# Performance work log

Measured on AMD Instinct MI355X. Metric: run time of the kernel, lower is better.

Reference implementation:

```python
import jax, jax.numpy as jnp
import numpy as np
import math

B, M, D = 16, 2048, 512
H, K, NB = 8, 5, 5
HD = D // H
FF = 2048


def _p(key, shape, scale=0.02):
    return (jax.random.normal(key, shape, dtype=jnp.float32) * scale)


def setup_inputs() -> dict:
    key = jax.random.key(0)
    ks = jax.random.split(key, 16)
    inp = {
        'x': jax.random.normal(ks[0], (B, M, D), dtype=jnp.float32),
        'mask': jnp.ones((B, 1, M), dtype=bool),
        'ln1_g': jnp.ones((D,), jnp.float32), 'ln1_b': jnp.zeros((D,), jnp.float32),
        'Wk': _p(ks[1], (D, D)), 'bk': jnp.zeros((D,), jnp.float32),
        'Wv': _p(ks[2], (D, D)), 'bv': jnp.zeros((D,), jnp.float32),
        'Wq': _p(ks[3], (D, D)), 'bq': jnp.zeros((D,), jnp.float32),
        'Woff': _p(ks[4], (D, H * K)), 'boff': jnp.zeros((H * K,), jnp.float32),
        'Wo': _p(ks[5], (D, D)), 'bo': jnp.zeros((D,), jnp.float32),
        'ln2_g': jnp.ones((D,), jnp.float32), 'ln2_b': jnp.zeros((D,), jnp.float32),
        'W1': _p(ks[6], (D, FF)), 'b1': jnp.zeros((FF,), jnp.float32),
        'W2': _p(ks[7], (FF, D)), 'b2': jnp.zeros((D,), jnp.float32),
    }
    return inp


def layer_norm(x, g, b, eps=1e-6):
    mu = jnp.mean(x, axis=-1, keepdims=True)
    var = jnp.mean((x - mu) ** 2, axis=-1, keepdims=True)
    return (x - mu) / jnp.sqrt(var + eps) * g + b


def grid_sample_1d(src, gx):
    # src: [BH, Min, hd], gx: [BH, M, K] normalized x-coords in [-1,1]
    # Replicates torch grid_sample(bilinear, zeros, align_corners=False) with
    # H_in=1 and y-grid==1 -> implicit 0.5 factor from y-interp against zero pad.
    BH, Min, hd = src.shape
    ix = ((gx + 1.0) * Min - 1.0) / 2.0
    x0 = jnp.floor(ix)
    w1 = ix - x0
    x0i = x0.astype(jnp.int32)

    def gather(xi):
        valid = ((xi >= 0) & (xi < Min)).astype(src.dtype)
        xc = jnp.clip(xi, 0, Min - 1)
        flat = xc.reshape(BH, -1)
        vals = jnp.take_along_axis(src, flat[:, :, None], axis=1)
        return vals.reshape(BH, xi.shape[1], xi.shape[2], hd) * valid[..., None]

    v0 = gather(x0i)
    v1 = gather(x0i + 1)
    return ((1.0 - w1)[..., None] * v0 + w1[..., None] * v1) * 0.5


def reference(x, mask, ln1_g, ln1_b, Wk, bk, Wv, bv, Wq, bq, Woff, boff,
              Wo, bo, ln2_g, ln2_b, W1, b1, W2, b2):
    Bs, Ms, Ds = x.shape
    xn = layer_norm(x, ln1_g, ln1_b)
    k = xn @ Wk + bk
    v = xn @ Wv + bv
    q = xn @ Wq + bq

    # query_type == 'mean': AvgPool1d(kernel=NB, stride=1, pad=NB//2),
    # count_include_pad=True -> moving sum over zero-padded seq / NB
    pad = NB // 2
    qp = jnp.pad(q, ((0, 0), (pad, pad), (0, 0)))
    cs = jnp.concatenate([jnp.zeros((Bs, 1, Ds), q.dtype), jnp.cumsum(qp, axis=1)], axis=1)
    q = (cs[:, NB:, :] - cs[:, :-NB, :]) / float(NB)  # [B, M, D]

    offsets = (q @ Woff + boff).reshape(Bs, Ms, H, K).transpose(0, 2, 1, 3)  # [B,H,M,K]
    kh = k.reshape(Bs, Ms, H, HD).transpose(0, 2, 1, 3)  # [B,H,M,hd]
    vh = v.reshape(Bs, Ms, H, HD).transpose(0, 2, 1, 3)
    qh = q.reshape(Bs, Ms, H, HD).transpose(0, 2, 1, 3)

    loc = jnp.arange(Ms, dtype=jnp.float32)[:, None]          # [M,1]
    left = -K // 2                                            # Python floor div: -3 for K=5
    ref = jnp.arange(left, K + left, dtype=jnp.float32)       # [K]
    sign_lens = jnp.squeeze(jnp.sum(mask, axis=-1)).astype(jnp.float32) - 1.0  # [B]

    sl = ref + offsets + loc                                  # [B,H,M,K]
    sl = jnp.mod(sl, sign_lens[:, None, None, None])
    gx = (sl / (Ms - 1) * 2.0 - 1.0).reshape(Bs * H, Ms, K)

    ksrc = kh.reshape(Bs * H, Ms, HD)
    vsrc = vh.reshape(Bs * H, Ms, HD)
    sk = grid_sample_1d(ksrc, gx).reshape(Bs, H, Ms, K, HD)
    sv = grid_sample_1d(vsrc, gx).reshape(Bs, H, Ms, K, HD)

    qh = qh / math.sqrt(HD)
    scores = jnp.einsum('bhmd,bhmkd->bhmk', qh, sk)
    attn = jax.nn.softmax(scores, axis=-1)
    ctx = jnp.einsum('bhmk,bhmkd->bhmd', attn, sv)
    ctx = ctx.transpose(0, 2, 1, 3).reshape(Bs, Ms, H * HD)
    att_out = ctx @ Wo + bo

    o = att_out + x  # dropout=0.0
    on = layer_norm(o, ln2_g, ln2_b)
    ff = jax.nn.relu(on @ W1 + b1) @ W2 + b2
    return ff + o
```

## Files before the change

### kernel.cpp

```cpp
#include <hip/hip_runtime.h>


#define B_   16
#define M_   2048
#define D_   512
#define H_   8
#define K_   5
#define HD_  64
#define FF_  2048
#define NROWS (B_ * M_)

typedef unsigned short u16;
typedef __attribute__((ext_vector_type(4))) unsigned short u16x4;
typedef __attribute__((ext_vector_type(8))) unsigned short u16x8;
typedef __attribute__((ext_vector_type(8))) short short8;
typedef __attribute__((ext_vector_type(4))) float f32x4;

__device__ __forceinline__ u16 f2bf(float f) {
  unsigned u = __builtin_bit_cast(unsigned, f);
  u += 0x7fff + ((u >> 16) & 1);
  return (u16)(u >> 16);
}
__device__ __forceinline__ float bf2f(u16 h) {
  unsigned u = (unsigned)h << 16;
  return __builtin_bit_cast(float, u);
}

#define GLP(p)  ((__attribute__((address_space(1))) void*)(p))
#define LDSP(p) ((__attribute__((address_space(3))) void*)(p))

__global__ __launch_bounds__(256)
void wtrans(const float* __restrict__ in, int K, int N,
            u16* __restrict__ out, int padN) {
  __shared__ float t[32][33];
  const int tx = threadIdx.x, ty = threadIdx.y;
  const int n0 = blockIdx.x * 32, k0 = blockIdx.y * 32;
#pragma unroll
  for (int r = 0; r < 4; ++r) {
    const int k = k0 + ty + r * 8;
    const int n = n0 + tx;
    t[ty + r * 8][tx] = (n < N) ? in[(size_t)k * N + n] : 0.f;
  }
  __syncthreads();
#pragma unroll
  for (int r = 0; r < 4; ++r) {
    const int nn = n0 + ty + r * 8;
    out[(size_t)nn * K + k0 + tx] = f2bf(t[tx][ty + r * 8]);
  }
}

__global__ __launch_bounds__(256)
void kvperm(const u16* __restrict__ tmp, u16* __restrict__ out) {
  const int g = blockIdx.x * 256 + threadIdx.x;
  const int row = g >> 6, j = g & 63;
  const int h = row >> 7, r = row & 127;
  const int src = ((r >> 2) & 1) * 512 + h * 64 + (r >> 3) * 4 + (r & 3);
  *(u16x8*)&out[(size_t)row * 512 + j * 8] =
      *(const u16x8*)&tmp[(size_t)src * 512 + j * 8];
}

__global__ __launch_bounds__(256)
void bias_cat(const float* __restrict__ bk, const float* __restrict__ bv,
              const float* __restrict__ bq, float* __restrict__ o) {
  const int i = blockIdx.x * 256 + threadIdx.x;
  if (i >= 1024) { o[i] = bq[i - 1024]; return; }
  const int h = i >> 7, r = i & 127;
  const int c = h * 64 + (r >> 3) * 4 + (r & 3);
  o[i] = ((r >> 2) & 1) ? bv[c] : bk[c];
}

__global__ __launch_bounds__(128)
void ln_bf16(const float* __restrict__ x, const float* __restrict__ g,
             const float* __restrict__ bsh, u16* __restrict__ y) {
  const int row = blockIdx.x;
  float4 v = ((const float4*)(x + (size_t)row * D_))[threadIdx.x];
  float s  = v.x + v.y + v.z + v.w;
  float s2 = v.x * v.x + v.y * v.y + v.z * v.z + v.w * v.w;
#pragma unroll
  for (int off = 32; off; off >>= 1) {
    s  += __shfl_xor(s, off);
    s2 += __shfl_xor(s2, off);
  }
  __shared__ float sh[4];
  if ((threadIdx.x & 63) == 0) {
    sh[threadIdx.x >> 6]       = s;
    sh[2 + (threadIdx.x >> 6)] = s2;
  }
  __syncthreads();
  s = sh[0] + sh[1]; s2 = sh[2] + sh[3];
  const float mu  = s * (1.0f / D_);
  const float var = s2 * (1.0f / D_) - mu * mu;
  const float inv = rsqrtf(var + 1e-6f);
  float4 gv = ((const float4*)g)[threadIdx.x];
  float4 bv = ((const float4*)bsh)[threadIdx.x];
  u16x4 o;
  o.x = f2bf((v.x - mu) * inv * gv.x + bv.x);
  o.y = f2bf((v.y - mu) * inv * gv.y + bv.y);
  o.z = f2bf((v.z - mu) * inv * gv.z + bv.z);
  o.w = f2bf((v.w - mu) * inv * gv.w + bv.w);
  *(u16x4*)(y + (size_t)row * D_ + threadIdx.x * 4) = o;
}

__global__ __launch_bounds__(128)
void ln_bf16_in(const u16* __restrict__ x, const float* __restrict__ g,
                const float* __restrict__ bsh, u16* __restrict__ y) {
  const int row = blockIdx.x;
  u16x4 hv = *(const u16x4*)(x + (size_t)row * D_ + threadIdx.x * 4);
  float4 v;
  v.x = bf2f(hv.x); v.y = bf2f(hv.y); v.z = bf2f(hv.z); v.w = bf2f(hv.w);
  float s  = v.x + v.y + v.z + v.w;
  float s2 = v.x * v.x + v.y * v.y + v.z * v.z + v.w * v.w;
#pragma unroll
  for (int off = 32; off; off >>= 1) {
    s  += __shfl_xor(s, off);
    s2 += __shfl_xor(s2, off);
  }
  __shared__ float sh[4];
  if ((threadIdx.x & 63) == 0) {
    sh[threadIdx.x >> 6]       = s;
    sh[2 + (threadIdx.x >> 6)] = s2;
  }
  __syncthreads();
  s = sh[0] + sh[1]; s2 = sh[2] + sh[3];
  const float mu  = s * (1.0f / D_);
  const float var = s2 * (1.0f / D_) - mu * mu;
  const float inv = rsqrtf(var + 1e-6f);
  float4 gv = ((const float4*)g)[threadIdx.x];
  float4 bv = ((const float4*)bsh)[threadIdx.x];
  u16x4 o;
  o.x = f2bf((v.x - mu) * inv * gv.x + bv.x);
  o.y = f2bf((v.y - mu) * inv * gv.y + bv.y);
  o.z = f2bf((v.z - mu) * inv * gv.z + bv.z);
  o.w = f2bf((v.w - mu) * inv * gv.w + bv.w);
  *(u16x4*)(y + (size_t)row * D_ + threadIdx.x * 4) = o;
}

template<int EPI, int OUTBF, int RBF>
__global__ __launch_bounds__(512, 2)
void mgemmS(const u16* __restrict__ A, int lda,
            const u16* __restrict__ Wt, int ldb, int Kdim,
            const float* __restrict__ bias,
            const void* R, int ldr,
            void* Cv, int ldc, int Ncols, int nbx) {
  __shared__ u16 lds[81920] __attribute__((aligned(128)));
  int bid = blockIdx.x;
  { const int q = (int)gridDim.x >> 3; bid = (bid & 7) * q + (bid >> 3); }
  const int bx = bid % nbx, by = bid / nbx;
  const int m0 = by * 256, n0 = bx * 256;

  const int tid  = threadIdx.x;
  const int w    = tid >> 6, lane = tid & 63;
  const int wr   = w >> 2,   wc   = w & 3;
  const int lr   = lane & 15, kg  = lane >> 4;
  const int NT   = Kdim >> 6;
  const int srow = (w << 3) + (lane >> 3);
  const int scol = (((lane & 7) ^ (lane >> 3)) << 3);

  const u16* Ab = A  + (size_t)m0 * lda;
  const u16* Bb = Wt + (size_t)n0 * ldb;

  auto stage = [&](const u16* gbase, int ld, int kt, int h, int base) {
    const u16* s0 = gbase + (size_t)(h * 128 + srow) * ld + kt * 64 + scol;
    const u16* s1 = s0 + (size_t)64 * ld;
    u16* d0 = &lds[base + h * 8192 + w * 512];
    __builtin_amdgcn_global_load_lds(GLP(s0), LDSP(d0),        16, 0, 0);
    __builtin_amdgcn_global_load_lds(GLP(s1), LDSP(d0 + 4096), 16, 0, 0);
  };
  auto rdA = [&](int base, int f, int s) -> short8 {
    const int row = wr * 128 + f * 16 + lr;
    const int cb  = (kg * 16 + s * 64) ^ ((lr & 7) << 4);
    return *(const short8*)&lds[base + row * 64 + (cb >> 1)];
  };
  auto rdB = [&](int bsel, int nn, int s) -> short8 {
    const int row = wc * 64 + nn * 16 + lr;
    const int cb  = (kg * 16 + s * 64) ^ ((lr & 7) << 4);
    return *(const short8*)&lds[49152 + bsel * 16384 + row * 64 + (cb >> 1)];
  };

  f32x4 acc[8][4];
#pragma unroll
  for (int f = 0; f < 8; ++f)
#pragma unroll
    for (int n = 0; n < 4; ++n) acc[f][n] = (f32x4){0.f, 0.f, 0.f, 0.f};

  stage(Ab, lda, 0, 0, 0);      stage(Ab, lda, 0, 1, 0);
  stage(Bb, ldb, 0, 0, 49152);  stage(Bb, ldb, 0, 1, 49152);
  if (NT > 1) {
    stage(Ab, lda, 1, 0, 16384);  stage(Ab, lda, 1, 1, 16384);
    stage(Bb, ldb, 1, 0, 65536);  stage(Bb, ldb, 1, 1, 65536);
    asm volatile("s_waitcnt vmcnt(8)" ::: "memory");
  } else {
    asm volatile("s_waitcnt vmcnt(0)" ::: "memory");
  }
  asm volatile("s_barrier" ::: "memory");

  int aCur = 0, bCur = 0;
  for (int t = 0; t < NT; ++t) {
    int aT2 = aCur + 2; if (aT2 >= 3) aT2 -= 3;
    const int aBase = aCur * 16384;
    const int aT2b  = aT2 * 16384;
    const int bT2b  = 49152 + bCur * 16384;
    short8 bfr[4][2];
    short8 afr[2][2][2];
#pragma unroll
    for (int n = 0; n < 4; ++n) { bfr[n][0] = rdB(bCur, n, 0); bfr[n][1] = rdB(bCur, n, 1); }
#pragma unroll
    for (int i = 0; i < 2; ++i) { afr[0][i][0] = rdA(aBase, i, 0); afr[0][i][1] = rdA(aBase, i, 1); }
    if (t + 2 < NT) { stage(Ab, lda, t + 2, 0, aT2b); stage(Ab, lda, t + 2, 1, aT2b); }
#pragma unroll
    for (int q = 0; q < 4; ++q) {
      if (q < 3) {
#pragma unroll
        for (int i = 0; i < 2; ++i) {
          afr[(q + 1) & 1][i][0] = rdA(aBase, 2 * (q + 1) + i, 0);
          afr[(q + 1) & 1][i][1] = rdA(aBase, 2 * (q + 1) + i, 1);
        }
      }
#pragma unroll
      for (int i = 0; i < 2; ++i)
#pragma unroll
        for (int n = 0; n < 4; ++n) {
          acc[2 * q + i][n] = __builtin_amdgcn_mfma_f32_16x16x32_bf16(afr[q & 1][i][0], bfr[n][0], acc[2 * q + i][n], 0, 0, 0);
          acc[2 * q + i][n] = __builtin_amdgcn_mfma_f32_16x16x32_bf16(afr[q & 1][i][1], bfr[n][1], acc[2 * q + i][n], 0, 0, 0);
        }
      if (q == 0) {
        asm volatile("s_waitcnt lgkmcnt(8)" ::: "memory");
        asm volatile("s_barrier" ::: "memory");
        if (t + 2 < NT) { stage(Bb, ldb, t + 2, 0, bT2b); stage(Bb, ldb, t + 2, 1, bT2b); }
      }
    }
    if (t + 1 < NT) {
      if (t + 2 < NT) { asm volatile("s_waitcnt vmcnt(8) lgkmcnt(0)" ::: "memory"); }
      else            { asm volatile("s_waitcnt vmcnt(0) lgkmcnt(0)" ::: "memory"); }
      asm volatile("s_barrier" ::: "memory");
    }
    aCur = (aCur + 1 < 3) ? aCur + 1 : 0;
    bCur ^= 1;
  }

  float* eplds = (float*)lds;
  asm volatile("s_waitcnt vmcnt(0) lgkmcnt(0)" ::: "memory");
  __builtin_amdgcn_s_barrier();
  const int ccol = lane * 4;
  float4 bb4 = make_float4(0.f, 0.f, 0.f, 0.f);
  if (n0 + ccol < Ncols) bb4 = *(const float4*)(bias + n0 + ccol);
#pragma unroll
  for (int half = 0; half < 2; ++half) {
#pragma unroll
    for (int fl = 0; fl < 4; ++fl) {
      const int f  = half * 4 + fl;
      const int cr = (fl * 2 + wr) * 16 + kg * 4;
#pragma unroll
      for (int n = 0; n < 4; ++n)
#pragma unroll
        for (int r = 0; r < 4; ++r)
          eplds[(cr + r) * 260 + wc * 64 + n * 16 + lr] = acc[f][n][r];
    }
    asm volatile("s_waitcnt lgkmcnt(0)" ::: "memory");
    __builtin_amdgcn_s_barrier();
#pragma unroll
    for (int i = 0; i < 16; ++i) {
      const int cr  = w * 16 + i;
      const int fl2 = cr >> 5, wr2 = (cr >> 4) & 1, r16 = cr & 15;
      const int grow = m0 + wr2 * 128 + (half * 4 + fl2) * 16 + r16;
      const int gcol = n0 + ccol;
      if (gcol < Ncols) {
        float4 v = *(const float4*)&eplds[cr * 260 + ccol];
        v.x += bb4.x; v.y += bb4.y; v.z += bb4.z; v.w += bb4.w;
        if (EPI == 1) {
          if (RBF) {
            u16x4 rv = *(const u16x4*)((const u16*)R + (size_t)grow * ldr + gcol);
            v.x += bf2f(rv.x); v.y += bf2f(rv.y); v.z += bf2f(rv.z); v.w += bf2f(rv.w);
          } else {
            float4 rv = *(const float4*)((const float*)R + (size_t)grow * ldr + gcol);
            v.x += rv.x; v.y += rv.y; v.z += rv.z; v.w += rv.w;
          }
        }
        if (EPI == 2) {
          v.x = fmaxf(v.x, 0.f); v.y = fmaxf(v.y, 0.f);
          v.z = fmaxf(v.z, 0.f); v.w = fmaxf(v.w, 0.f);
        }
        if (OUTBF) {
          u16x4 o;
          o.x = f2bf(v.x); o.y = f2bf(v.y); o.z = f2bf(v.z); o.w = f2bf(v.w);
          *(u16x4*)((u16*)Cv + (size_t)grow * ldc + gcol) = o;
        } else {
          *(float4*)((float*)Cv + (size_t)grow * ldc + gcol) = v;
        }
      }
    }
    if (half == 0) {
      asm volatile("s_waitcnt lgkmcnt(0)" ::: "memory");
      __builtin_amdgcn_s_barrier();
    }
  }
}

__global__ __launch_bounds__(256)
void pool_q_bf(const u16* __restrict__ kvq, u16* __restrict__ qp) {
  const size_t idx = (size_t)blockIdx.x * 256 + threadIdx.x;
  const int d4 = (int)(idx & 127);
  const size_t bm = idx >> 7;
  const int m = (int)(bm & (M_ - 1));
  float a0 = 0.f, a1 = 0.f, a2 = 0.f, a3 = 0.f;
#pragma unroll
  for (int j = -2; j <= 2; ++j) {
    const int mm = m + j;
    if (mm >= 0 && mm < M_) {
      u16x4 tv = *(const u16x4*)(kvq + (bm + j) * 1536 + 1024 + d4 * 4);
      a0 += bf2f(tv.x); a1 += bf2f(tv.y); a2 += bf2f(tv.z); a3 += bf2f(tv.w);
    }
  }
  u16x4 o;
  o.x = f2bf(a0 * 0.2f); o.y = f2bf(a1 * 0.2f);
  o.z = f2bf(a2 * 0.2f); o.w = f2bf(a3 * 0.2f);
  *(u16x4*)(qp + bm * D_ + d4 * 4) = o;
}

__global__ __launch_bounds__(256)
void attn3(const u16* __restrict__ KVQ, const u16* __restrict__ QP,
           const float* __restrict__ OFFS, u16* __restrict__ CTX) {
  const int tid  = threadIdx.x;
  const int lane = tid & 63;
  const int j    = lane & 7;
  const int grp  = lane >> 3;
  const int gid  = blockIdx.x * 32 + (tid >> 6) * 8 + grp;
  const int m  = gid & (M_ - 1);
  const int bh = gid >> 11;
  const int h  = bh & (H_ - 1);
  const int b  = bh >> 3;
  const size_t bm = (size_t)b * M_ + m;

  float qs[8];
  {
    u16x8 qv = *(const u16x8*)(QP + bm * D_ + h * HD_ + j * 8);
#pragma unroll
    for (int e = 0; e < 8; ++e) qs[e] = bf2f(qv[e]) * 0.0625f;
  }
  const float* ob = OFFS + bm * (H_ * K_) + h * K_;
  const u16* kvb = KVQ + h * 128 + j * 16;
  const size_t rowb = (size_t)b * M_;

  float sc[K_], sv[K_][8];
#pragma unroll
  for (int kk = 0; kk < K_; ++kk) {
    float sl = (float)(m + kk - 3) + ob[kk];
    if (sl < 0.f) sl += 2047.f;
    else if (sl >= 2047.f) sl -= 2047.f;
    const float ix  = sl * (2048.0f / 2047.0f) - 0.5f;
    const float x0f = floorf(ix);
    const float w1  = ix - x0f;
    const int   x0  = (int)x0f;
    u16x8 a0, b0, a1, b1;
#pragma unroll
    for (int e = 0; e < 8; ++e) { a0[e] = 0; b0[e] = 0; a1[e] = 0; b1[e] = 0; }
    if (x0 >= 0) {
      const u16* p = kvb + (rowb + x0) * 1536;
      a0 = *(const u16x8*)p; b0 = *(const u16x8*)(p + 8);
    }
    if (x0 < M_ - 1) {
      const u16* p = kvb + (rowb + x0 + 1) * 1536;
      a1 = *(const u16x8*)p; b1 = *(const u16x8*)(p + 8);
    }
    float part = 0.f;
#pragma unroll
    for (int e = 0; e < 4; ++e) {
      const float k0 = bf2f(a0[e]),     k1 = bf2f(a1[e]);
      const float v0 = bf2f(a0[e + 4]), v1 = bf2f(a1[e + 4]);
      part += (k0 + w1 * (k1 - k0)) * qs[e];
      sv[kk][e] = v0 + w1 * (v1 - v0);
      const float k0b = bf2f(b0[e]),     k1b = bf2f(b1[e]);
      const float v0b = bf2f(b0[e + 4]), v1b = bf2f(b1[e + 4]);
      part += (k0b + w1 * (k1b - k0b)) * qs[e + 4];
      sv[kk][e + 4] = v0b + w1 * (v1b - v0b);
    }
    part += __shfl_xor(part, 1);
    part += __shfl_xor(part, 2);
    part += __shfl_xor(part, 4);
    sc[kk] = part;
  }
  float mx = sc[0];
#pragma unroll
  for (int kk = 1; kk < K_; ++kk) mx = fmaxf(mx, sc[kk]);
  float den = 0.f;
#pragma unroll
  for (int kk = 0; kk < K_; ++kk) { sc[kk] = __expf(sc[kk] - mx); den += sc[kk]; }
  const float inv = 1.0f / den;
  float c[8] = {0, 0, 0, 0, 0, 0, 0, 0};
#pragma unroll
  for (int kk = 0; kk < K_; ++kk) {
    const float wgt = sc[kk] * inv;
#pragma unroll
    for (int e = 0; e < 8; ++e) c[e] += wgt * sv[kk][e];
  }
  u16x8 o;
#pragma unroll
  for (int e = 0; e < 8; ++e) o[e] = f2bf(c[e] * 0.5f);
  *(u16x8*)(CTX + bm * 1536 + h * HD_ + j * 8) = o;
}

extern "C" void kernel_launch(void* const* d_in, const int* in_sizes, int n_in,
                              void* d_out, int out_size, void* d_ws, size_t ws_size,
                              hipStream_t stream) {
  const float* x     = (const float*)d_in[0];
  const float* ln1_g = (const float*)d_in[2];
  const float* ln1_b = (const float*)d_in[3];
  const float* Wk    = (const float*)d_in[4];
  const float* bk    = (const float*)d_in[5];
  const float* Wv    = (const float*)d_in[6];
  const float* bv    = (const float*)d_in[7];
  const float* Wq    = (const float*)d_in[8];
  const float* bq    = (const float*)d_in[9];
  const float* Woff  = (const float*)d_in[10];
  const float* boff  = (const float*)d_in[11];
  const float* Wo    = (const float*)d_in[12];
  const float* bo    = (const float*)d_in[13];
  const float* ln2_g = (const float*)d_in[14];
  const float* ln2_b = (const float*)d_in[15];
  const float* W1    = (const float*)d_in[16];
  const float* b1    = (const float*)d_in[17];
  const float* W2    = (const float*)d_in[18];
  const float* b2    = (const float*)d_in[19];
  float* out = (float*)d_out;

  if (ws_size < 181403648ull) return;
  char* ws = (char*)d_ws;
  u16* WKVQt = (u16*)ws;
  u16* Wot   = (u16*)(ws + 1572864ull);
  u16* Wofft = (u16*)(ws + 2097152ull);
  u16* W1t   = (u16*)(ws + 2359296ull);
  u16* W2t   = (u16*)(ws + 4456448ull);
  float* BKVQ = (float*)(ws + 6553600ull);
  u16* TMPKV = (u16*)(ws + 6559744ull);
  u16*  XN   = (u16*)(ws + 8388608ull);
  float* OFFS = (float*)(ws + 41943040ull);
  u16*  OB   = (u16*)(ws + 47185920ull);
  u16*  KVQ  = (u16*)(ws + 80740352ull);
  u16*  HIDc = KVQ;

  const dim3 tb(32, 8);
  wtrans<<<dim3(16, 16), tb, 0, stream>>>(Wk, 512, 512, TMPKV,          512);
  wtrans<<<dim3(16, 16), tb, 0, stream>>>(Wv, 512, 512, TMPKV + 262144, 512);
  kvperm<<<256, 256, 0, stream>>>(TMPKV, WKVQt);
  wtrans<<<dim3(16, 16), tb, 0, stream>>>(Wq, 512, 512, WKVQt + 524288, 512);
  wtrans<<<dim3(16, 16), tb, 0, stream>>>(Wo, 512, 512, Wot, 512);
  wtrans<<<dim3(8, 16),  tb, 0, stream>>>(Woff, 512, 40, Wofft, 256);
  wtrans<<<dim3(64, 16), tb, 0, stream>>>(W1, 512, 2048, W1t, 2048);
  wtrans<<<dim3(16, 64), tb, 0, stream>>>(W2, 2048, 512, W2t, 512);
  bias_cat<<<6, 256, 0, stream>>>(bk, bv, bq, BKVQ);

  ln_bf16<<<NROWS, 128, 0, stream>>>(x, ln1_g, ln1_b, XN);
  mgemmS<0,1,0><<<768, 512, 0, stream>>>(XN, 512, WKVQt, 512, 512, BKVQ,
                                         nullptr, 0, KVQ, 1536, 1536, 6);
  pool_q_bf<<<16384, 256, 0, stream>>>(KVQ, XN);
  mgemmS<0,0,0><<<128, 512, 0, stream>>>(XN, 512, Wofft, 512, 512, boff,
                                         nullptr, 0, OFFS, 40, 40, 1);
  attn3<<<8192, 256, 0, stream>>>(KVQ, XN, OFFS, KVQ + 1024);
  mgemmS<1,1,0><<<256, 512, 0, stream>>>(KVQ + 1024, 1536, Wot, 512, 512, bo,
                                         x, 512, OB, 512, 512, 2);
  ln_bf16_in<<<NROWS, 128, 0, stream>>>(OB, ln2_g, ln2_b, XN);
  for (int c = 0; c < 2; ++c) {
    const size_t ro = (size_t)c * 16384 * 512;
    mgemmS<2,1,0><<<512, 512, 0, stream>>>(XN + ro, 512, W1t, 512, 512, b1,
                                           nullptr, 0, HIDc, 2048, 2048, 8);
    mgemmS<1,0,1><<<128, 512, 0, stream>>>(HIDc, 2048, W2t, 2048, 2048, b2,
                                           OB + ro, 512, out + ro, 512, 512, 2);
  }
}
```

Baseline: 420.2 us.

## Replace 256x256 LDS-staged GEMM with 128x128 tile reading A directly from global

The GEMM moves from 256x256 tiles with 512 threads, where both A and B are staged through a triple/double-buffered LDS ring, to 128x128 tiles with 256 threads. Only B is staged through LDS, and A fragments are loaded straight from global memory into registers every K step. The aim is lower LDS use, more blocks for occupancy and better load balance, and a simpler barrier schedule. The cost is lower data reuse per tile, uncoalesced 16-byte global reads of A that depend on cache hits, and global load latency exposed just before the MFMAs.

```diff
diff --git a/kernel.cpp b/kernel.cpp
--- a/kernel.cpp
+++ b/kernel.cpp
@@ -136,136 +136,112 @@
 }
 
 template<int EPI, int OUTBF, int RBF>
-__global__ __launch_bounds__(512, 2)
-void mgemmS(const u16* __restrict__ A, int lda,
+__global__ __launch_bounds__(256)
+void mgemmG(const u16* __restrict__ A, int lda,
             const u16* __restrict__ Wt, int ldb, int Kdim,
             const float* __restrict__ bias,
             const void* R, int ldr,
             void* Cv, int ldc, int Ncols, int nbx) {
-  __shared__ u16 lds[81920] __attribute__((aligned(128)));
+  __shared__ u16 lds[16896] __attribute__((aligned(128)));
   int bid = blockIdx.x;
   { const int q = (int)gridDim.x >> 3; bid = (bid & 7) * q + (bid >> 3); }
   const int bx = bid % nbx, by = bid / nbx;
-  const int m0 = by * 256, n0 = bx * 256;
+  const int m0 = by * 128, n0 = bx * 128;
 
   const int tid  = threadIdx.x;
   const int w    = tid >> 6, lane = tid & 63;
-  const int wr   = w >> 2,   wc   = w & 3;
+  const int wwr  = w >> 1,   wwc  = w & 1;
   const int lr   = lane & 15, kg  = lane >> 4;
   const int NT   = Kdim >> 6;
-  const int srow = (w << 3) + (lane >> 3);
-  const int scol = (((lane & 7) ^ (lane >> 3)) << 3);
-
-  const u16* Ab = A  + (size_t)m0 * lda;
-  const u16* Bb = Wt + (size_t)n0 * ldb;
-
-  auto stage = [&](const u16* gbase, int ld, int kt, int h, int base) {
-    const u16* s0 = gbase + (size_t)(h * 128 + srow) * ld + kt * 64 + scol;
-    const u16* s1 = s0 + (size_t)64 * ld;
-    u16* d0 = &lds[base + h * 8192 + w * 512];
-    __builtin_amdgcn_global_load_lds(GLP(s0), LDSP(d0),        16, 0, 0);
-    __builtin_amdgcn_global_load_lds(GLP(s1), LDSP(d0 + 4096), 16, 0, 0);
-  };
-  auto rdA = [&](int base, int f, int s) -> short8 {
-    const int row = wr * 128 + f * 16 + lr;
-    const int cb  = (kg * 16 + s * 64) ^ ((lr & 7) << 4);
-    return *(const short8*)&lds[base + row * 64 + (cb >> 1)];
+
+  const u16* Bb   = Wt + (size_t)n0 * ldb;
+  const u16* Arow = A + (size_t)(m0 + wwr * 64 + lr) * lda + kg * 8;
+  const size_t fstep = (size_t)16 * lda;
+
+  auto stageB = [&](int kt, int bsel) {
+#pragma unroll
+    for (int l = 0; l < 4; ++l) {
+      const int row = l * 32 + (tid >> 3);
+      const int ce  = ((tid & 7) * 8) ^ ((row & 7) * 8);
+      const u16* s = Bb + (size_t)row * ldb + kt * 64 + ce;
+      u16* d = &lds[bsel * 8192 + l * 2048 + tid * 8];
+      __builtin_amdgcn_global_load_lds(GLP(s), LDSP(d), 16, 0, 0);
+    }
   };
   auto rdB = [&](int bsel, int nn, int s) -> short8 {
-    const int row = wc * 64 + nn * 16 + lr;
+    const int row = wwc * 64 + nn * 16 + lr;
     const int cb  = (kg * 16 + s * 64) ^ ((lr & 7) << 4);
-    return *(const short8*)&lds[49152 + bsel * 16384 + row * 64 + (cb >> 1)];
+    return *(const short8*)&lds[bsel * 8192 + row * 64 + (cb >> 1)];
   };
 
-  f32x4 acc[8][4];
-#pragma unroll
-  for (int f = 0; f < 8; ++f)
+  f32x4 acc[4][4];
+#pragma unroll
+  for (int f = 0; f < 4; ++f)
 #pragma unroll
     for (int n = 0; n < 4; ++n) acc[f][n] = (f32x4){0.f, 0.f, 0.f, 0.f};
 
-  stage(Ab, lda, 0, 0, 0);      stage(Ab, lda, 0, 1, 0);
-  stage(Bb, ldb, 0, 0, 49152);  stage(Bb, ldb, 0, 1, 49152);
+  stageB(0, 0);
   if (NT > 1) {
-    stage(Ab, lda, 1, 0, 16384);  stage(Ab, lda, 1, 1, 16384);
-    stage(Bb, ldb, 1, 0, 65536);  stage(Bb, ldb, 1, 1, 65536);
-    asm volatile("s_waitcnt vmcnt(8)" ::: "memory");
+    stageB(1, 1);
+    asm volatile("s_waitcnt vmcnt(4)" ::: "memory");
   } else {
     asm volatile("s_waitcnt vmcnt(0)" ::: "memory");
   }
-  asm volatile("s_barrier" ::: "memory");
-
-  int aCur = 0, bCur = 0;
+  __builtin_amdgcn_s_barrier();
+
+  int bCur = 0;
   for (int t = 0; t < NT; ++t) {
-    int aT2 = aCur + 2; if (aT2 >= 3) aT2 -= 3;
-    const int aBase = aCur * 16384;
-    const int aT2b  = aT2 * 16384;
-    const int bT2b  = 49152 + bCur * 16384;
-    short8 bfr[4][2];
-    short8 afr[2][2][2];
+    short8 bfr[4][2], afr[4][2];
 #pragma unroll
     for (int n = 0; n < 4; ++n) { bfr[n][0] = rdB(bCur, n, 0); bfr[n][1] = rdB(bCur, n, 1); }
-#pragma unroll
-    for (int i = 0; i < 2; ++i) { afr[0][i][0] = rdA(aBase, i, 0); afr[0][i][1] = rdA(aBase, i, 1); }
-    if (t + 2 < NT) { stage(Ab, lda, t + 2, 0, aT2b); stage(Ab, lda, t + 2, 1, aT2b); }
-#pragma unroll
-    for (int q = 0; q < 4; ++q) {
-      if (q < 3) {
-#pragma unroll
-        for (int i = 0; i < 2; ++i) {
-          afr[(q + 1) & 1][i][0] = rdA(aBase, 2 * (q + 1) + i, 0);
-          afr[(q + 1) & 1][i][1] = rdA(aBase, 2 * (q + 1) + i, 1);
-        }
+    const u16* At = Arow + (size_t)t * 64;
+#pragma unroll
+    for (int f = 0; f < 4; ++f) {
+      afr[f][0] = *(const short8*)(At + (size_t)f * fstep);
+      afr[f][1] = *(const short8*)(At + (size_t)f * fstep + 32);
+    }
+    asm volatile("s_waitcnt lgkmcnt(0)" ::: "memory");
+    __builtin_amdgcn_s_barrier();
+    __builtin_amdgcn_sched_barrier(0);
+    if (t + 2 < NT) stageB(t + 2, bCur);
+#pragma unroll
+    for (int f = 0; f < 4; ++f)
+#pragma unroll
+      for (int n = 0; n < 4; ++n) {
+        acc[f][n] = __builtin_amdgcn_mfma_f32_16x16x32_bf16(afr[f][0], bfr[n][0], acc[f][n], 0, 0, 0);
+        acc[f][n] = __builtin_amdgcn_mfma_f32_16x16x32_bf16(afr[f][1], bfr[n][1], acc[f][n], 0, 0, 0);
       }
-#pragma unroll
-      for (int i = 0; i < 2; ++i)
-#pragma unroll
-        for (int n = 0; n < 4; ++n) {
-          acc[2 * q + i][n] = __builtin_amdgcn_mfma_f32_16x16x32_bf16(afr[q & 1][i][0], bfr[n][0], acc[2 * q + i][n], 0, 0, 0);
-          acc[2 * q + i][n] = __builtin_amdgcn_mfma_f32_16x16x32_bf16(afr[q & 1][i][1], bfr[n][1], acc[2 * q + i][n], 0, 0, 0);
-        }
-      if (q == 0) {
-        asm volatile("s_waitcnt lgkmcnt(8)" ::: "memory");
-        asm volatile("s_barrier" ::: "memory");
-        if (t + 2 < NT) { stage(Bb, ldb, t + 2, 0, bT2b); stage(Bb, ldb, t + 2, 1, bT2b); }
-      }
-    }
-    if (t + 1 < NT) {
-      if (t + 2 < NT) { asm volatile("s_waitcnt vmcnt(8) lgkmcnt(0)" ::: "memory"); }
-      else            { asm volatile("s_waitcnt vmcnt(0) lgkmcnt(0)" ::: "memory"); }
-      asm volatile("s_barrier" ::: "memory");
-    }
-    aCur = (aCur + 1 < 3) ? aCur + 1 : 0;
+    __builtin_amdgcn_s_barrier();
     bCur ^= 1;
   }
 
   float* eplds = (float*)lds;
   asm volatile("s_waitcnt vmcnt(0) lgkmcnt(0)" ::: "memory");
   __builtin_amdgcn_s_barrier();
-  const int ccol = lane * 4;
+  const int ccol = (tid & 31) * 4;
+  const int crr  = tid >> 5;
   float4 bb4 = make_float4(0.f, 0.f, 0.f, 0.f);
   if (n0 + ccol < Ncols) bb4 = *(const float4*)(bias + n0 + ccol);
 #pragma unroll
-  for (int half = 0; half < 2; ++half) {
-#pragma unroll
-    for (int fl = 0; fl < 4; ++fl) {
-      const int f  = half * 4 + fl;
-      const int cr = (fl * 2 + wr) * 16 + kg * 4;
-#pragma unroll
-      for (int n = 0; n < 4; ++n)
-#pragma unroll
-        for (int r = 0; r < 4; ++r)
-          eplds[(cr + r) * 260 + wc * 64 + n * 16 + lr] = acc[f][n][r];
+  for (int h = 0; h < 2; ++h) {
+    if (wwr == h) {
+#pragma unroll
+      for (int f = 0; f < 4; ++f)
+#pragma unroll
+        for (int n = 0; n < 4; ++n)
+#pragma unroll
+          for (int r = 0; r < 4; ++r)
+            eplds[(f * 16 + kg * 4 + r) * 132 + wwc * 64 + n * 16 + lr] = acc[f][n][r];
     }
     asm volatile("s_waitcnt lgkmcnt(0)" ::: "memory");
     __builtin_amdgcn_s_barrier();
 #pragma unroll
-    for (int i = 0; i < 16; ++i) {
-      const int cr  = w * 16 + i;
-      const int fl2 = cr >> 5, wr2 = (cr >> 4) & 1, r16 = cr & 15;
-      const int grow = m0 + wr2 * 128 + (half * 4 + fl2) * 16 + r16;
+    for (int i = 0; i < 8; ++i) {
+      const int cr   = i * 8 + crr;
+      const int grow = m0 + h * 64 + cr;
       const int gcol = n0 + ccol;
       if (gcol < Ncols) {
-        float4 v = *(const float4*)&eplds[cr * 260 + ccol];
+        float4 v = *(const float4*)&eplds[cr * 132 + ccol];
         v.x += bb4.x; v.y += bb4.y; v.z += bb4.z; v.w += bb4.w;
         if (EPI == 1) {
           if (RBF) {
@@ -289,7 +265,7 @@
         }
       }
     }
-    if (half == 0) {
+    if (h == 0) {
       asm volatile("s_waitcnt lgkmcnt(0)" ::: "memory");
       __builtin_amdgcn_s_barrier();
     }
@@ -450,20 +426,20 @@
   bias_cat<<<6, 256, 0, stream>>>(bk, bv, bq, BKVQ);
 
   ln_bf16<<<NROWS, 128, 0, stream>>>(x, ln1_g, ln1_b, XN);
-  mgemmS<0,1,0><<<768, 512, 0, stream>>>(XN, 512, WKVQt, 512, 512, BKVQ,
-                                         nullptr, 0, KVQ, 1536, 1536, 6);
+  mgemmG<0,1,0><<<3072, 256, 0, stream>>>(XN, 512, WKVQt, 512, 512, BKVQ,
+                                          nullptr, 0, KVQ, 1536, 1536, 12);
   pool_q_bf<<<16384, 256, 0, stream>>>(KVQ, XN);
-  mgemmS<0,0,0><<<128, 512, 0, stream>>>(XN, 512, Wofft, 512, 512, boff,
-                                         nullptr, 0, OFFS, 40, 40, 1);
+  mgemmG<0,0,0><<<512, 256, 0, stream>>>(XN, 512, Wofft, 512, 512, boff,
+                                         nullptr, 0, OFFS, 40, 40, 2);
   attn3<<<8192, 256, 0, stream>>>(KVQ, XN, OFFS, KVQ + 1024);
-  mgemmS<1,1,0><<<256, 512, 0, stream>>>(KVQ + 1024, 1536, Wot, 512, 512, bo,
-                                         x, 512, OB, 512, 512, 2);
+  mgemmG<1,1,0><<<1024, 256, 0, stream>>>(KVQ + 1024, 1536, Wot, 512, 512, bo,
+                                          x, 512, OB, 512, 512, 4);
   ln_bf16_in<<<NROWS, 128, 0, stream>>>(OB, ln2_g, ln2_b, XN);
   for (int c = 0; c < 2; ++c) {
     const size_t ro = (size_t)c * 16384 * 512;
-    mgemmS<2,1,0><<<512, 512, 0, stream>>>(XN + ro, 512, W1t, 512, 512, b1,
-                                           nullptr, 0, HIDc, 2048, 2048, 8);
-    mgemmS<1,0,1><<<128, 512, 0, stream>>>(HIDc, 2048, W2t, 2048, 2048, b2,
-                                           OB + ro, 512, out + ro, 512, 512, 2);
-  }
-}
+    mgemmG<2,1,0><<<2048, 256, 0, stream>>>(XN + ro, 512, W1t, 512, 512, b1,
+                                            nullptr, 0, HIDc, 2048, 2048, 16);
+    mgemmG<1,0,1><<<512, 256, 0, stream>>>(HIDc, 2048, W2t, 2048, 2048, b2,
+                                           OB + ro, 512, out + ro, 512, 512, 4);
+  }
+}
```

Result: slower. 609.7 us (+45.1%).
